# Kernel tuning notes

Hardware: AMD Instinct MI355X
Metric: run time of the kernel (lower is better)

Reference implementation:

```python
import jax, jax.numpy as jnp
import numpy as np

B, NL, C, H, W = 4, 2048, 128, 128, 128
N_PTS0, N_PTS1 = 32, 8
SCALE = N_PTS0 // N_PTS1  # MaxPool1d kernel/stride
FEATURE_DIM = 5
BN_EPS = 1e-5


def setup_inputs() -> dict:
    key = jax.random.key(0)
    ks = jax.random.split(key, 12)
    fm = jax.random.normal(ks[0], (B, C, H, W), dtype=jnp.float32)
    lines = jax.random.uniform(ks[1], (B, NL, 2, 2), dtype=jnp.float32) * 128.0
    P = C // 2
    s = 0.05
    return {
        "feature_map": fm,
        "lines": lines,
        # Bottleneck1D params (BatchNorm in eval mode: running_mean=0, running_var=1)
        "bn1_g": jnp.ones((C,), jnp.float32), "bn1_b": jnp.zeros((C,), jnp.float32),
        "conv1_w": jax.random.normal(ks[2], (P, C, 1), jnp.float32) * s,
        "conv1_b": jnp.zeros((P,), jnp.float32),
        "bn2_g": jnp.ones((P,), jnp.float32), "bn2_b": jnp.zeros((P,), jnp.float32),
        "conv2_w": jax.random.normal(ks[3], (P, P, 3), jnp.float32) * s,
        "conv2_b": jnp.zeros((P,), jnp.float32),
        "bn3_g": jnp.ones((P,), jnp.float32), "bn3_b": jnp.zeros((P,), jnp.float32),
        "conv3_w": jax.random.normal(ks[4], (C, P, 1), jnp.float32) * s,
        "conv3_b": jnp.zeros((C,), jnp.float32),
        # fc2: ReLU -> Linear(dim_loi*n_pts1 + 5, 4)
        "fc2_w": jax.random.normal(ks[5], (4, C * N_PTS1 + FEATURE_DIM), jnp.float32) * s,
        "fc2_b": jnp.zeros((4,), jnp.float32),
    }


def _bn(x, g, b):
    # eval-mode BatchNorm1d with running_mean=0, running_var=1
    return x * (g / jnp.sqrt(1.0 + BN_EPS))[None, :, None] + b[None, :, None]


def _conv1d(x, w, b, pad):
    y = jax.lax.conv_general_dilated(x, w, (1,), [(pad, pad)],
                                     dimension_numbers=("NCH", "OIH", "NCH"))
    return y + b[None, :, None]


def _loi_gather(fm, lines):
    # sample points along each line: [B, NL, N_PTS0, 2]
    lam = jnp.linspace(0.0, 1.0, N_PTS0, dtype=jnp.float32)[None, None, :, None]
    p = lines[:, :, 0:1, :] * lam + lines[:, :, 1:2, :] * (1.0 - lam) - 0.5
    p = p.reshape(B, -1, 2)                      # [B, NL*N_PTS0, 2]
    px, py = p[..., 0], p[..., 1]
    px0 = jnp.clip(jnp.floor(px), 0.0, 127.0)
    py0 = jnp.clip(jnp.floor(py), 0.0, 127.0)
    px1 = jnp.clip(px0 + 1.0, 0.0, 127.0)
    py1 = jnp.clip(py0 + 1.0, 0.0, 127.0)
    px0l, py0l = px0.astype(jnp.int32), py0.astype(jnp.int32)
    px1l, py1l = px1.astype(jnp.int32), py1.astype(jnp.int32)

    gather = jax.vmap(lambda f, yi, xi: f[:, yi, xi])  # [C, P] per image
    # weights exactly as in the torch source
    xp = (gather(fm, py0l, px0l) * ((px1 - px) * (py1 - py))[:, None, :]
          + gather(fm, py1l, px0l) * ((px - px0) * (py1 - py))[:, None, :]
          + gather(fm, py0l, px1l) * ((px1 - px) * (py - py0))[:, None, :]
          + gather(fm, py1l, px1l) * ((px - px0) * (py - py0))[:, None, :])
    # [B, C, NL*N_PTS0] -> [B*NL, C, N_PTS0]
    xp = xp.reshape(B, C, NL, N_PTS0).transpose(0, 2, 1, 3).reshape(B * NL, C, N_PTS0)
    return xp


def reference(feature_map, lines, bn1_g, bn1_b, conv1_w, conv1_b,
              bn2_g, bn2_b, conv2_w, conv2_b, bn3_g, bn3_b,
              conv3_w, conv3_b, fc2_w, fc2_b):
    xp = _loi_gather(feature_map, lines)               # [B*NL, C, N_PTS0]
    # MaxPool1d(SCALE, SCALE)
    x = xp.reshape(B * NL, C, N_PTS1, SCALE).max(axis=-1)
    # Bottleneck1D residual block
    y = jax.nn.relu(_bn(x, bn1_g, bn1_b))
    y = _conv1d(y, conv1_w, conv1_b, 0)
    y = jax.nn.relu(_bn(y, bn2_g, bn2_b))
    y = _conv1d(y, conv2_w, conv2_b, 1)
    y = jax.nn.relu(_bn(y, bn3_g, bn3_b))
    y = _conv1d(y, conv3_w, conv3_b, 0)
    x = x + y                                          # [B*NL, C, N_PTS1]
    # line geometry feature (use_cood=1, use_slop=1)
    xyu, xyv = lines[:, :, 0, :], lines[:, :, 1, :]
    u2v = jnp.sqrt(((xyu - xyv) ** 2).sum(-1, keepdims=True)).clip(min=1e-6)
    f = jnp.concatenate([xyu / 128.0, xyv / 128.0, u2v], axis=-1)
    f = f.reshape(B * NL, FEATURE_DIM)
    # concat + fc2 (ReLU -> Linear)
    x = jnp.concatenate([x.reshape(B * NL, C * N_PTS1), f], axis=1)
    logits = jax.nn.relu(x) @ fc2_w.T + fc2_b
    prob = jax.nn.softmax(logits, axis=1)
    return logits, prob
```

## Files before the change

### kernel.cpp

```cpp
#include <hip/hip_runtime.h>
#include <math.h>

#define BB 4
#define NLL 2048
#define CC 128
#define HH 128
#define WW 128
#define NPTS0 32
#define NPTS1 8
#define PP 64
#define FDIM 5
#define FCK (CC*NPTS1 + FDIM)

typedef __attribute__((ext_vector_type(8))) short bf16x8;
typedef __attribute__((ext_vector_type(4))) float f32x4;

__device__ __forceinline__ unsigned short f2bf(float f) {
    union { float f; unsigned u; } v; v.f = f;
    unsigned u = v.u;
    return (unsigned short)((u + 0x7fffu + ((u >> 16) & 1u)) >> 16);
}

__global__ __launch_bounds__(256)
void transpose_fm2(const float* __restrict__ fm, float* __restrict__ fmT) {
    __shared__ float tile[32 * 132];
    const int c0 = blockIdx.x * 32;
    const int by = blockIdx.y;
    const int b = by >> 7, y = by & 127;
    const int t = threadIdx.x;
    const float* src = fm + ((size_t)b * CC) * (HH * WW) + (size_t)y * WW;
    const int x4 = (t & 31) * 4;
    #pragma unroll
    for (int i = 0; i < 4; ++i) {
        int r = (t >> 5) + 8 * i;
        *(float4*)&tile[r * 132 + x4] =
            *(const float4*)&src[(size_t)(c0 + r) * (HH * WW) + x4];
    }
    __syncthreads();
    float* dst = fmT + (size_t)by * WW * CC + c0 + (t & 31);
    const int cr = (t & 31) * 132;
    #pragma unroll
    for (int i = 0; i < 16; ++i) {
        int x = (t >> 5) + 8 * i;
        dst[(size_t)x * CC] = tile[cr + x];
    }
}

__global__ __launch_bounds__(256)
void prep_weights(const float* __restrict__ w1, const float* __restrict__ w2,
                  const float* __restrict__ w3, unsigned short* __restrict__ W1b,
                  unsigned short* __restrict__ W2b, unsigned short* __restrict__ W3b) {
    int gid = blockIdx.x * 256 + threadIdx.x;
    if (gid < 8192) {
        W1b[gid] = f2bf(w1[gid]);
    } else if (gid < 20480) {
        int g = gid - 8192;
        int tt = g >> 12, r = g & 4095;
        int p = r >> 6, q = r & 63;
        W2b[tt * 4096 + p * 64 + q] = f2bf(w2[p * 192 + q * 3 + tt]);
    } else if (gid < 28672) {
        int g = gid - 20480;
        W3b[g] = f2bf(w3[g]);
    }
}

__global__ __launch_bounds__(256)
void line_mfma(const float* __restrict__ fmT,
               const float* __restrict__ lines,
               const float* __restrict__ bn1_g, const float* __restrict__ bn1_b,
               const unsigned short* __restrict__ W1b, const float* __restrict__ b1,
               const float* __restrict__ bn2_g, const float* __restrict__ bn2_b,
               const unsigned short* __restrict__ W2b, const float* __restrict__ b2,
               const float* __restrict__ bn3_g, const float* __restrict__ bn3_b,
               const unsigned short* __restrict__ W3b, const float* __restrict__ b3,
               const float* __restrict__ fcw,   const float* __restrict__ fcb,
               float* __restrict__ out) {
    __shared__ int   s_ix0[64], s_ix1[64], s_iy0[64], s_iy1[64];
    __shared__ float s_wA[64], s_wB[64], s_wC[64], s_wD[64];
    __shared__ float s_xs[16 * 128];
    __shared__ unsigned short s_ybn[16 * 136];
    __shared__ unsigned short s_z1[2 * 10 * 72];
    __shared__ unsigned short s_z2[16 * 72];
    __shared__ float s_feat[2][8];
    __shared__ float s_red[4 * 8];

    const int bx  = blockIdx.x;
    const int L0  = bx * 2;
    const int b   = bx >> 10;
    const int tid = threadIdx.x;
    const int lane = tid & 63;
    const int wv   = tid >> 6;
    const int quad = lane >> 4;
    const int l16  = lane & 15;
    const float inv_s = 1.0f / sqrtf(1.0f + 1e-5f);

    if (tid < 64) {
        int line = tid >> 5, pt = tid & 31;
        const float* ln = lines + (size_t)(L0 + line) * 4;
        float lam = (float)pt * (1.0f / 31.0f);
        float om  = 1.0f - lam;
        float px = ln[0] * lam + ln[2] * om - 0.5f;
        float py = ln[1] * lam + ln[3] * om - 0.5f;
        float px0 = fminf(fmaxf(floorf(px), 0.0f), 127.0f);
        float py0 = fminf(fmaxf(floorf(py), 0.0f), 127.0f);
        float px1 = fminf(px0 + 1.0f, 127.0f);
        float py1 = fminf(py0 + 1.0f, 127.0f);
        s_ix0[tid] = (int)px0; s_ix1[tid] = (int)px1;
        s_iy0[tid] = (int)py0; s_iy1[tid] = (int)py1;
        float ax = px1 - px, bxv = px - px0, ay = py1 - py, byv = py - py0;
        s_wA[tid] = ax  * ay;
        s_wB[tid] = bxv * ay;
        s_wC[tid] = ax  * byv;
        s_wD[tid] = bxv * byv;
    }
    if (tid >= 64 && tid < 66) {
        int line = tid - 64;
        const float* ln = lines + (size_t)(L0 + line) * 4;
        float ux = ln[0], uy = ln[1], vx = ln[2], vy = ln[3];
        float dx = ux - vx, dy = uy - vy;
        float d = fmaxf(sqrtf(dx * dx + dy * dy), 1e-6f);
        s_feat[line][0] = ux * (1.0f / 128.0f);
        s_feat[line][1] = uy * (1.0f / 128.0f);
        s_feat[line][2] = vx * (1.0f / 128.0f);
        s_feat[line][3] = vy * (1.0f / 128.0f);
        s_feat[line][4] = d;
    }
    if (tid < 128) {
        int line = tid >> 6, q = tid & 63;
        s_z1[line * 720 + 0 * 72 + q] = 0;
        s_z1[line * 720 + 9 * 72 + q] = 0;
    }
    __syncthreads();

    {
        int cq = tid & 31, k = tid >> 5;
        int c0 = cq * 4;
        const float* base = fmT + (size_t)b * (HH * WW * CC);
        #pragma unroll
        for (int line = 0; line < 2; ++line) {
            float4 acc;
            acc.x = -INFINITY; acc.y = -INFINITY; acc.z = -INFINITY; acc.w = -INFINITY;
            #pragma unroll
            for (int j = 0; j < 4; ++j) {
                int pt = line * 32 + k * 4 + j;
                int ix0 = s_ix0[pt], ix1 = s_ix1[pt];
                int iy0 = s_iy0[pt], iy1 = s_iy1[pt];
                float wA = s_wA[pt], wB = s_wB[pt], wC = s_wC[pt], wD = s_wD[pt];
                float4 vA = *(const float4*)(base + ((size_t)(iy0 * WW + ix0)) * CC + c0);
                float4 vB = *(const float4*)(base + ((size_t)(iy1 * WW + ix0)) * CC + c0);
                float4 vC = *(const float4*)(base + ((size_t)(iy0 * WW + ix1)) * CC + c0);
                float4 vD = *(const float4*)(base + ((size_t)(iy1 * WW + ix1)) * CC + c0);
                float4 v;
                v.x = wA * vA.x + wB * vB.x + wC * vC.x + wD * vD.x;
                v.y = wA * vA.y + wB * vB.y + wC * vC.y + wD * vD.y;
                v.z = wA * vA.z + wB * vB.z + wC * vC.z + wD * vD.z;
                v.w = wA * vA.w + wB * vB.w + wC * vC.w + wD * vD.w;
                acc.x = fmaxf(acc.x, v.x); acc.y = fmaxf(acc.y, v.y);
                acc.z = fmaxf(acc.z, v.z); acc.w = fmaxf(acc.w, v.w);
            }
            *(float4*)&s_xs[(line * 8 + k) * 128 + c0] = acc;
        }
    }
    __syncthreads();

    {
        int m = tid >> 4, c8 = (tid & 15) * 8;
        const float* xr = &s_xs[m * 128 + c8];
        float4 g0 = *(const float4*)(bn1_g + c8);
        float4 g1 = *(const float4*)(bn1_g + c8 + 4);
        float4 bb0 = *(const float4*)(bn1_b + c8);
        float4 bb1 = *(const float4*)(bn1_b + c8 + 4);
        const float* gg = (const float*)&g0;
        float gs[8] = {g0.x, g0.y, g0.z, g0.w, g1.x, g1.y, g1.z, g1.w};
        float bs[8] = {bb0.x, bb0.y, bb0.z, bb0.w, bb1.x, bb1.y, bb1.z, bb1.w};
        (void)gg;
        unsigned short* yr = &s_ybn[m * 136 + c8];
        #pragma unroll
        for (int i = 0; i < 8; ++i) {
            float v = fmaxf(xr[i] * (gs[i] * inv_s) + bs[i], 0.0f);
            yr[i] = f2bf(v);
        }
    }
    __syncthreads();

    {
        int n0 = wv * 16;
        f32x4 acc = {0.f, 0.f, 0.f, 0.f};
        #pragma unroll
        for (int kc = 0; kc < 4; ++kc) {
            bf16x8 a = *(const bf16x8*)&s_ybn[l16 * 136 + kc * 32 + quad * 8];
            bf16x8 bf = *(const bf16x8*)(W1b + (n0 + l16) * 128 + kc * 32 + quad * 8);
            acc = __builtin_amdgcn_mfma_f32_16x16x32_bf16(a, bf, acc, 0, 0, 0);
        }
        int p = n0 + l16;
        float s2 = bn2_g[p] * inv_s, bb2 = bn2_b[p], cb = b1[p];
        int line = quad >> 1;
        int kbase = (quad & 1) * 4;
        #pragma unroll
        for (int r = 0; r < 4; ++r) {
            float v = fmaxf((acc[r] + cb) * s2 + bb2, 0.0f);
            s_z1[line * 720 + (kbase + r + 1) * 72 + p] = f2bf(v);
        }
    }
    __syncthreads();

    {
        int n0 = wv * 16;
        f32x4 acc = {0.f, 0.f, 0.f, 0.f};
        int line = l16 >> 3, k = l16 & 7;
        #pragma unroll
        for (int t = 0; t < 3; ++t) {
            const unsigned short* arow = &s_z1[line * 720 + (k + t) * 72];
            #pragma unroll
            for (int kc = 0; kc < 2; ++kc) {
                bf16x8 a = *(const bf16x8*)&arow[kc * 32 + quad * 8];
                bf16x8 bf = *(const bf16x8*)(W2b + t * 4096 + (n0 + l16) * 64 + kc * 32 + quad * 8);
                acc = __builtin_amdgcn_mfma_f32_16x16x32_bf16(a, bf, acc, 0, 0, 0);
            }
        }
        int p = n0 + l16;
        float s3 = bn3_g[p] * inv_s, bb3 = bn3_b[p], cb = b2[p];
        #pragma unroll
        for (int r = 0; r < 4; ++r) {
            float v = fmaxf((acc[r] + cb) * s3 + bb3, 0.0f);
            s_z2[(quad * 4 + r) * 72 + p] = f2bf(v);
        }
    }
    __syncthreads();

    float p0 = 0.f, p1 = 0.f, p2 = 0.f, p3 = 0.f;
    {
        int kbase = (quad & 1) * 4;
        bf16x8 a0 = *(const bf16x8*)&s_z2[l16 * 72 + 0 * 32 + quad * 8];
        bf16x8 a1 = *(const bf16x8*)&s_z2[l16 * 72 + 1 * 32 + quad * 8];
        #pragma unroll
        for (int sub = 0; sub < 2; ++sub) {
            int n0 = wv * 32 + sub * 16;
            f32x4 acc = {0.f, 0.f, 0.f, 0.f};
            bf16x8 bf0 = *(const bf16x8*)(W3b + (n0 + l16) * 64 + 0 * 32 + quad * 8);
            bf16x8 bf1 = *(const bf16x8*)(W3b + (n0 + l16) * 64 + 1 * 32 + quad * 8);
            acc = __builtin_amdgcn_mfma_f32_16x16x32_bf16(a0, bf0, acc, 0, 0, 0);
            acc = __builtin_amdgcn_mfma_f32_16x16x32_bf16(a1, bf1, acc, 0, 0, 0);
            int c = n0 + l16;
            float cb = b3[c];
            #pragma unroll
            for (int r = 0; r < 4; ++r) {
                int m = quad * 4 + r;
                float v = fmaxf(s_xs[m * 128 + c] + acc[r] + cb, 0.0f);
                int idx = c * 8 + kbase + r;
                p0 = fmaf(v, fcw[0 * FCK + idx], p0);
                p1 = fmaf(v, fcw[1 * FCK + idx], p1);
                p2 = fmaf(v, fcw[2 * FCK + idx], p2);
                p3 = fmaf(v, fcw[3 * FCK + idx], p3);
            }
        }
    }
    #pragma unroll
    for (int off = 16; off >= 1; off >>= 1) {
        p0 += __shfl_down(p0, off);
        p1 += __shfl_down(p1, off);
        p2 += __shfl_down(p2, off);
        p3 += __shfl_down(p3, off);
    }
    if ((lane & 31) == 0) {
        int line = lane >> 5;
        s_red[wv * 8 + line * 4 + 0] = p0;
        s_red[wv * 8 + line * 4 + 1] = p1;
        s_red[wv * 8 + line * 4 + 2] = p2;
        s_red[wv * 8 + line * 4 + 3] = p3;
    }
    __syncthreads();

    if (tid < 2) {
        int line = tid;
        float lg[4];
        #pragma unroll
        for (int o = 0; o < 4; ++o) {
            lg[o] = fcb[o] + s_red[0 + line * 4 + o] + s_red[8 + line * 4 + o]
                  + s_red[16 + line * 4 + o] + s_red[24 + line * 4 + o];
        }
        #pragma unroll
        for (int j = 0; j < FDIM; ++j) {
            float fv = fmaxf(s_feat[line][j], 0.0f);
            #pragma unroll
            for (int o = 0; o < 4; ++o)
                lg[o] = fmaf(fv, fcw[o * FCK + 1024 + j], lg[o]);
        }
        float m = fmaxf(fmaxf(lg[0], lg[1]), fmaxf(lg[2], lg[3]));
        float e0 = expf(lg[0] - m), e1 = expf(lg[1] - m);
        float e2 = expf(lg[2] - m), e3 = expf(lg[3] - m);
        float inv = 1.0f / (e0 + e1 + e2 + e3);
        float* lo = out + (size_t)(L0 + line) * 4;
        lo[0] = lg[0]; lo[1] = lg[1]; lo[2] = lg[2]; lo[3] = lg[3];
        float* pr = out + (size_t)BB * NLL * 4 + (size_t)(L0 + line) * 4;
        pr[0] = e0 * inv; pr[1] = e1 * inv; pr[2] = e2 * inv; pr[3] = e3 * inv;
    }
}

template<bool TRANS>
__global__ __launch_bounds__(256)
void line_kernel_v1(const float* __restrict__ fm,
                    const float* __restrict__ lines,
                    const float* __restrict__ bn1_g, const float* __restrict__ bn1_b,
                    const float* __restrict__ w1,    const float* __restrict__ b1,
                    const float* __restrict__ bn2_g, const float* __restrict__ bn2_b,
                    const float* __restrict__ w2,    const float* __restrict__ b2,
                    const float* __restrict__ bn3_g, const float* __restrict__ bn3_b,
                    const float* __restrict__ w3,    const float* __restrict__ b3,
                    const float* __restrict__ fcw,   const float* __restrict__ fcb,
                    float* __restrict__ out) {
    __shared__ int   s_ix0[32], s_ix1[32], s_iy0[32], s_iy1[32];
    __shared__ float s_wA[32], s_wB[32], s_wC[32], s_wD[32];
    __shared__ float xs [8][132];
    __shared__ float ybn[8][132];
    __shared__ float z1 [64][12];
    __shared__ float z2 [64][8];
    __shared__ float s_feat[8];
    __shared__ float s_red[16];

    const int L   = blockIdx.x;
    const int b   = L / NLL;
    const int tid = threadIdx.x;
    const float inv_s = 1.0f / sqrtf(1.0f + 1e-5f);
    const float* ln = lines + (size_t)L * 4;

    if (tid < 32) {
        float lam = (float)tid * (1.0f / 31.0f);
        float om  = 1.0f - lam;
        float px = ln[0] * lam + ln[2] * om - 0.5f;
        float py = ln[1] * lam + ln[3] * om - 0.5f;
        float px0 = fminf(fmaxf(floorf(px), 0.0f), 127.0f);
        float py0 = fminf(fmaxf(floorf(py), 0.0f), 127.0f);
        float px1 = fminf(px0 + 1.0f, 127.0f);
        float py1 = fminf(py0 + 1.0f, 127.0f);
        s_ix0[tid] = (int)px0; s_ix1[tid] = (int)px1;
        s_iy0[tid] = (int)py0; s_iy1[tid] = (int)py1;
        float ax = px1 - px, bxv = px - px0, ay = py1 - py, byv = py - py0;
        s_wA[tid] = ax  * ay;  s_wB[tid] = bxv * ay;
        s_wC[tid] = ax  * byv; s_wD[tid] = bxv * byv;
    }
    if (tid == 0) {
        float ux = ln[0], uy = ln[1], vx = ln[2], vy = ln[3];
        float dx = ux - vx, dy = uy - vy;
        float d = fmaxf(sqrtf(dx * dx + dy * dy), 1e-6f);
        s_feat[0] = ux / 128.0f; s_feat[1] = uy / 128.0f;
        s_feat[2] = vx / 128.0f; s_feat[3] = vy / 128.0f;
        s_feat[4] = d;
    }
    __syncthreads();
    {
        int cq = tid & 31, k = tid >> 5, c0 = cq * 4;
        float4 acc;
        acc.x = -INFINITY; acc.y = -INFINITY; acc.z = -INFINITY; acc.w = -INFINITY;
        #pragma unroll
        for (int j = 0; j < 4; ++j) {
            int pt = k * 4 + j;
            int ix0 = s_ix0[pt], ix1 = s_ix1[pt];
            int iy0 = s_iy0[pt], iy1 = s_iy1[pt];
            float wA = s_wA[pt], wB = s_wB[pt], wC = s_wC[pt], wD = s_wD[pt];
            float4 vA, vB, vC, vD;
            if (TRANS) {
                const float* base = fm + (size_t)b * HH * WW * CC;
                vA = *(const float4*)(base + ((size_t)(iy0 * WW + ix0)) * CC + c0);
                vB = *(const float4*)(base + ((size_t)(iy1 * WW + ix0)) * CC + c0);
                vC = *(const float4*)(base + ((size_t)(iy0 * WW + ix1)) * CC + c0);
                vD = *(const float4*)(base + ((size_t)(iy1 * WW + ix1)) * CC + c0);
            } else {
                const float* base = fm + ((size_t)b * CC + c0) * HH * WW;
                int oA = iy0 * WW + ix0, oB = iy1 * WW + ix0;
                int oC = iy0 * WW + ix1, oD = iy1 * WW + ix1;
                vA.x = base[oA];           vB.x = base[oB];
                vC.x = base[oC];           vD.x = base[oD];
                vA.y = base[HH*WW + oA];   vB.y = base[HH*WW + oB];
                vC.y = base[HH*WW + oC];   vD.y = base[HH*WW + oD];
                vA.z = base[2*HH*WW + oA]; vB.z = base[2*HH*WW + oB];
                vC.z = base[2*HH*WW + oC]; vD.z = base[2*HH*WW + oD];
                vA.w = base[3*HH*WW + oA]; vB.w = base[3*HH*WW + oB];
                vC.w = base[3*HH*WW + oC]; vD.w = base[3*HH*WW + oD];
            }
            float4 v;
            v.x = wA * vA.x + wB * vB.x + wC * vC.x + wD * vD.x;
            v.y = wA * vA.y + wB * vB.y + wC * vC.y + wD * vD.y;
            v.z = wA * vA.z + wB * vB.z + wC * vC.z + wD * vD.z;
            v.w = wA * vA.w + wB * vB.w + wC * vC.w + wD * vD.w;
            acc.x = fmaxf(acc.x, v.x); acc.y = fmaxf(acc.y, v.y);
            acc.z = fmaxf(acc.z, v.z); acc.w = fmaxf(acc.w, v.w);
        }
        *(float4*)(&xs[k][c0]) = acc;
    }
    __syncthreads();
    for (int e = tid; e < 1024; e += 256) {
        int k = e >> 7, c = e & 127;
        ybn[k][c] = fmaxf(xs[k][c] * (bn1_g[c] * inv_s) + bn1_b[c], 0.0f);
    }
    __syncthreads();
    if (tid < 64) { z1[tid][0] = 0.0f; z1[tid][9] = 0.0f; }
    {
        int p = tid >> 2, kq = tid & 3;
        const float* wrow = w1 + p * 128;
        float a0a = 0.f, a0b = 0.f, a1a = 0.f, a1b = 0.f;
        #pragma unroll 8
        for (int c = 0; c < 128; c += 4) {
            float4 w  = *(const float4*)(wrow + c);
            float4 ya = *(const float4*)(&ybn[kq][c]);
            float4 yb = *(const float4*)(&ybn[kq + 4][c]);
            a0a = fmaf(w.x, ya.x, a0a); a0b = fmaf(w.y, ya.y, a0b);
            a0a = fmaf(w.z, ya.z, a0a); a0b = fmaf(w.w, ya.w, a0b);
            a1a = fmaf(w.x, yb.x, a1a); a1b = fmaf(w.y, yb.y, a1b);
            a1a = fmaf(w.z, yb.z, a1a); a1b = fmaf(w.w, yb.w, a1b);
        }
        float s2 = bn2_g[p] * inv_s, bb = bn2_b[p], cb = b1[p];
        z1[p][1 + kq]     = fmaxf((a0a + a0b + cb) * s2 + bb, 0.0f);
        z1[p][1 + kq + 4] = fmaxf((a1a + a1b + cb) * s2 + bb, 0.0f);
    }
    __syncthreads();
    {
        int p = tid >> 2, kq = tid & 3;
        const float* wrow = w2 + p * 192;
        float acc0 = 0.f, acc1 = 0.f;
        #pragma unroll 4
        for (int q = 0; q < 64; ++q) {
            float w0 = wrow[q * 3 + 0], w1v = wrow[q * 3 + 1], w2v = wrow[q * 3 + 2];
            const float* zr = &z1[q][0];
            acc0 = fmaf(w0, zr[kq], acc0);
            acc0 = fmaf(w1v, zr[kq + 1], acc0);
            acc0 = fmaf(w2v, zr[kq + 2], acc0);
            acc1 = fmaf(w0, zr[kq + 4], acc1);
            acc1 = fmaf(w1v, zr[kq + 5], acc1);
            acc1 = fmaf(w2v, zr[kq + 6], acc1);
        }
        float s3 = bn3_g[p] * inv_s, bb = bn3_b[p], cb = b2[p];
        z2[p][kq]     = fmaxf((acc0 + cb) * s3 + bb, 0.0f);
        z2[p][kq + 4] = fmaxf((acc1 + cb) * s3 + bb, 0.0f);
    }
    __syncthreads();
    float part0 = 0.f, part1 = 0.f, part2 = 0.f, part3 = 0.f;
    {
        int c = tid >> 1, kq = tid & 1;
        const float* wrow = w3 + c * 64;
        float acc[4] = {0.f, 0.f, 0.f, 0.f};
        #pragma unroll 8
        for (int q = 0; q < 64; ++q) {
            float w = wrow[q];
            acc[0] = fmaf(w, z2[q][kq], acc[0]);
            acc[1] = fmaf(w, z2[q][kq + 2], acc[1]);
            acc[2] = fmaf(w, z2[q][kq + 4], acc[2]);
            acc[3] = fmaf(w, z2[q][kq + 6], acc[3]);
        }
        float cb = b3[c];
        #pragma unroll
        for (int i = 0; i < 4; ++i) {
            int k = kq + 2 * i;
            float v = fmaxf(xs[k][c] + acc[i] + cb, 0.0f);
            int idx = c * 8 + k;
            part0 = fmaf(v, fcw[0 * FCK + idx], part0);
            part1 = fmaf(v, fcw[1 * FCK + idx], part1);
            part2 = fmaf(v, fcw[2 * FCK + idx], part2);
            part3 = fmaf(v, fcw[3 * FCK + idx], part3);
        }
    }
    #pragma unroll
    for (int off = 32; off > 0; off >>= 1) {
        part0 += __shfl_down(part0, off);
        part1 += __shfl_down(part1, off);
        part2 += __shfl_down(part2, off);
        part3 += __shfl_down(part3, off);
    }
    if ((tid & 63) == 0) {
        int w = tid >> 6;
        s_red[w * 4 + 0] = part0; s_red[w * 4 + 1] = part1;
        s_red[w * 4 + 2] = part2; s_red[w * 4 + 3] = part3;
    }
    __syncthreads();
    if (tid == 0) {
        float lg[4];
        #pragma unroll
        for (int o = 0; o < 4; ++o)
            lg[o] = fcb[o] + s_red[o] + s_red[4 + o] + s_red[8 + o] + s_red[12 + o];
        #pragma unroll
        for (int j = 0; j < FDIM; ++j) {
            float fv = fmaxf(s_feat[j], 0.0f);
            #pragma unroll
            for (int o = 0; o < 4; ++o)
                lg[o] = fmaf(fv, fcw[o * FCK + 1024 + j], lg[o]);
        }
        float m = fmaxf(fmaxf(lg[0], lg[1]), fmaxf(lg[2], lg[3]));
        float e0 = expf(lg[0] - m), e1 = expf(lg[1] - m);
        float e2 = expf(lg[2] - m), e3 = expf(lg[3] - m);
        float inv = 1.0f / (e0 + e1 + e2 + e3);
        float* lo = out + (size_t)L * 4;
        lo[0] = lg[0]; lo[1] = lg[1]; lo[2] = lg[2]; lo[3] = lg[3];
        float* pr = out + (size_t)BB * NLL * 4 + (size_t)L * 4;
        pr[0] = e0 * inv; pr[1] = e1 * inv; pr[2] = e2 * inv; pr[3] = e3 * inv;
    }
}

extern "C" void kernel_launch(void* const* d_in, const int* in_sizes, int n_in,
                              void* d_out, int out_size, void* d_ws, size_t ws_size,
                              hipStream_t stream) {
    const float* fm     = (const float*)d_in[0];
    const float* lines  = (const float*)d_in[1];
    const float* bn1_g  = (const float*)d_in[2];
    const float* bn1_b  = (const float*)d_in[3];
    const float* w1     = (const float*)d_in[4];
    const float* b1     = (const float*)d_in[5];
    const float* bn2_g  = (const float*)d_in[6];
    const float* bn2_b  = (const float*)d_in[7];
    const float* w2     = (const float*)d_in[8];
    const float* b2     = (const float*)d_in[9];
    const float* bn3_g  = (const float*)d_in[10];
    const float* bn3_b  = (const float*)d_in[11];
    const float* w3     = (const float*)d_in[12];
    const float* b3     = (const float*)d_in[13];
    const float* fcw    = (const float*)d_in[14];
    const float* fcb    = (const float*)d_in[15];
    float* out = (float*)d_out;

    const size_t fmT_bytes = (size_t)BB * HH * WW * CC * sizeof(float);
    const size_t wb_bytes  = 57344;

    if (ws_size >= fmT_bytes + wb_bytes) {
        float* fmT = (float*)d_ws;
        unsigned short* W1b = (unsigned short*)((char*)d_ws + fmT_bytes);
        unsigned short* W2b = W1b + 8192;
        unsigned short* W3b = W2b + 12288;
        dim3 tg(CC / 32, BB * HH);
        transpose_fm2<<<tg, 256, 0, stream>>>(fm, fmT);
        prep_weights<<<112, 256, 0, stream>>>(w1, w2, w3, W1b, W2b, W3b);
        line_mfma<<<BB * NLL / 2, 256, 0, stream>>>(
            fmT, lines, bn1_g, bn1_b, W1b, b1, bn2_g, bn2_b, W2b, b2,
            bn3_g, bn3_b, W3b, b3, fcw, fcb, out);
    } else if (ws_size >= fmT_bytes) {
        float* fmT = (float*)d_ws;
        dim3 tg(CC / 32, BB * HH);
        transpose_fm2<<<tg, 256, 0, stream>>>(fm, fmT);
        line_kernel_v1<true><<<BB * NLL, 256, 0, stream>>>(
            fmT, lines, bn1_g, bn1_b, w1, b1, bn2_g, bn2_b, w2, b2,
            bn3_g, bn3_b, w3, b3, fcw, fcb, out);
    } else {
        line_kernel_v1<false><<<BB * NLL, 256, 0, stream>>>(
            fm, lines, bn1_g, bn1_b, w1, b1, bn2_g, bn2_b, w2, b2,
            bn3_g, bn3_b, w3, b3, fcw, fcb, out);
    }
}
```

Measured before the change: 167.4 us.

## Store transposed feature map in bf16 and gather 8-channel bf16 vectors

The transpose kernel now converts the feature map to bf16 while transposing to channel-last, using a swizzled shared tile and 64-column halves. The line kernel gathers bilinear corners as 8-wide bf16 vectors using precomputed flat offsets, then converts back to float for interpolation and max-pooling. This halves the bytes written by the transpose and read by the gather. The cost is reduced precision of the sampled features before pooling.

```diff
diff --git a/kernel.cpp b/kernel.cpp
--- a/kernel.cpp
+++ b/kernel.cpp
@@ -20,29 +20,41 @@
     unsigned u = v.u;
     return (unsigned short)((u + 0x7fffu + ((u >> 16) & 1u)) >> 16);
 }
+__device__ __forceinline__ float bf2f(unsigned short s) {
+    union { unsigned u; float f; } v; v.u = ((unsigned)s) << 16;
+    return v.f;
+}
 
 __global__ __launch_bounds__(256)
-void transpose_fm2(const float* __restrict__ fm, float* __restrict__ fmT) {
-    __shared__ float tile[32 * 132];
-    const int c0 = blockIdx.x * 32;
-    const int by = blockIdx.y;
+void transpose_fm3(const float* __restrict__ fm, unsigned short* __restrict__ fmT) {
+    __shared__ unsigned short tile[128 * 72];
+    const int by = blockIdx.x >> 1;
+    const int xh = blockIdx.x & 1;
     const int b = by >> 7, y = by & 127;
     const int t = threadIdx.x;
-    const float* src = fm + ((size_t)b * CC) * (HH * WW) + (size_t)y * WW;
-    const int x4 = (t & 31) * 4;
+    const float* src = fm + ((size_t)b * CC) * (HH * WW) + (size_t)y * WW + xh * 64;
+    const int x4 = (t & 15) * 4;
+    const int r0 = t >> 4;
     #pragma unroll
-    for (int i = 0; i < 4; ++i) {
-        int r = (t >> 5) + 8 * i;
-        *(float4*)&tile[r * 132 + x4] =
-            *(const float4*)&src[(size_t)(c0 + r) * (HH * WW) + x4];
-    }
-    __syncthreads();
-    float* dst = fmT + (size_t)by * WW * CC + c0 + (t & 31);
-    const int cr = (t & 31) * 132;
+    for (int i = 0; i < 8; ++i) {
+        int r = r0 + 16 * i;
+        float4 v = *(const float4*)&src[(size_t)r * (HH * WW) + x4];
+        ushort4 u;
+        u.x = f2bf(v.x); u.y = f2bf(v.y); u.z = f2bf(v.z); u.w = f2bf(v.w);
+        *(ushort4*)&tile[r * 72 + (x4 ^ (r & 28))] = u;
+    }
+    __syncthreads();
+    unsigned short* dst = fmT + ((size_t)by * WW + xh * 64) * CC;
+    const int c4 = (t & 31) * 4;
     #pragma unroll
-    for (int i = 0; i < 16; ++i) {
+    for (int i = 0; i < 8; ++i) {
         int x = (t >> 5) + 8 * i;
-        dst[(size_t)x * CC] = tile[cr + x];
+        ushort4 u;
+        u.x = tile[(c4 + 0) * 72 + (x ^ ((c4 + 0) & 28))];
+        u.y = tile[(c4 + 1) * 72 + (x ^ ((c4 + 1) & 28))];
+        u.z = tile[(c4 + 2) * 72 + (x ^ ((c4 + 2) & 28))];
+        u.w = tile[(c4 + 3) * 72 + (x ^ ((c4 + 3) & 28))];
+        *(ushort4*)&dst[(size_t)x * CC + c4] = u;
     }
 }
 
@@ -65,7 +77,7 @@
 }
 
 __global__ __launch_bounds__(256)
-void line_mfma(const float* __restrict__ fmT,
+void line_mfma(const unsigned short* __restrict__ fmT,
                const float* __restrict__ lines,
                const float* __restrict__ bn1_g, const float* __restrict__ bn1_b,
                const unsigned short* __restrict__ W1b, const float* __restrict__ b1,
@@ -75,7 +87,7 @@
                const unsigned short* __restrict__ W3b, const float* __restrict__ b3,
                const float* __restrict__ fcw,   const float* __restrict__ fcb,
                float* __restrict__ out) {
-    __shared__ int   s_ix0[64], s_ix1[64], s_iy0[64], s_iy1[64];
+    __shared__ int   s_oA[64], s_oB[64], s_oC[64], s_oD[64];
     __shared__ float s_wA[64], s_wB[64], s_wC[64], s_wD[64];
     __shared__ float s_xs[16 * 128];
     __shared__ unsigned short s_ybn[16 * 136];
@@ -105,8 +117,11 @@
         float py0 = fminf(fmaxf(floorf(py), 0.0f), 127.0f);
         float px1 = fminf(px0 + 1.0f, 127.0f);
         float py1 = fminf(py0 + 1.0f, 127.0f);
-        s_ix0[tid] = (int)px0; s_ix1[tid] = (int)px1;
-        s_iy0[tid] = (int)py0; s_iy1[tid] = (int)py1;
+        int ix0 = (int)px0, ix1 = (int)px1, iy0 = (int)py0, iy1 = (int)py1;
+        s_oA[tid] = (iy0 * WW + ix0) * CC;
+        s_oB[tid] = (iy1 * WW + ix0) * CC;
+        s_oC[tid] = (iy0 * WW + ix1) * CC;
+        s_oD[tid] = (iy1 * WW + ix1) * CC;
         float ax = px1 - px, bxv = px - px0, ay = py1 - py, byv = py - py0;
         s_wA[tid] = ax  * ay;
         s_wB[tid] = bxv * ay;
@@ -133,53 +148,46 @@
     __syncthreads();
 
     {
-        int cq = tid & 31, k = tid >> 5;
-        int c0 = cq * 4;
-        const float* base = fmT + (size_t)b * (HH * WW * CC);
-        #pragma unroll
-        for (int line = 0; line < 2; ++line) {
-            float4 acc;
-            acc.x = -INFINITY; acc.y = -INFINITY; acc.z = -INFINITY; acc.w = -INFINITY;
+        int tl = tid >> 4;
+        int line = tl >> 3, k = tl & 7;
+        int c8 = (tid & 15) * 8;
+        const unsigned short* base = fmT + (size_t)b * (HH * WW * CC) + c8;
+        float acc[8];
+        #pragma unroll
+        for (int i = 0; i < 8; ++i) acc[i] = -INFINITY;
+        #pragma unroll
+        for (int j = 0; j < 4; ++j) {
+            int pt = line * 32 + k * 4 + j;
+            bf16x8 rA = *(const bf16x8*)(base + s_oA[pt]);
+            bf16x8 rB = *(const bf16x8*)(base + s_oB[pt]);
+            bf16x8 rC = *(const bf16x8*)(base + s_oC[pt]);
+            bf16x8 rD = *(const bf16x8*)(base + s_oD[pt]);
+            float wA = s_wA[pt], wB = s_wB[pt], wC = s_wC[pt], wD = s_wD[pt];
             #pragma unroll
-            for (int j = 0; j < 4; ++j) {
-                int pt = line * 32 + k * 4 + j;
-                int ix0 = s_ix0[pt], ix1 = s_ix1[pt];
-                int iy0 = s_iy0[pt], iy1 = s_iy1[pt];
-                float wA = s_wA[pt], wB = s_wB[pt], wC = s_wC[pt], wD = s_wD[pt];
-                float4 vA = *(const float4*)(base + ((size_t)(iy0 * WW + ix0)) * CC + c0);
-                float4 vB = *(const float4*)(base + ((size_t)(iy1 * WW + ix0)) * CC + c0);
-                float4 vC = *(const float4*)(base + ((size_t)(iy0 * WW + ix1)) * CC + c0);
-                float4 vD = *(const float4*)(base + ((size_t)(iy1 * WW + ix1)) * CC + c0);
-                float4 v;
-                v.x = wA * vA.x + wB * vB.x + wC * vC.x + wD * vD.x;
-                v.y = wA * vA.y + wB * vB.y + wC * vC.y + wD * vD.y;
-                v.z = wA * vA.z + wB * vB.z + wC * vC.z + wD * vD.z;
-                v.w = wA * vA.w + wB * vB.w + wC * vC.w + wD * vD.w;
-                acc.x = fmaxf(acc.x, v.x); acc.y = fmaxf(acc.y, v.y);
-                acc.z = fmaxf(acc.z, v.z); acc.w = fmaxf(acc.w, v.w);
+            for (int i = 0; i < 8; ++i) {
+                float v = wA * bf2f((unsigned short)rA[i])
+                        + wB * bf2f((unsigned short)rB[i])
+                        + wC * bf2f((unsigned short)rC[i])
+                        + wD * bf2f((unsigned short)rD[i]);
+                acc[i] = fmaxf(acc[i], v);
             }
-            *(float4*)&s_xs[(line * 8 + k) * 128 + c0] = acc;
-        }
+        }
+        float* xr = &s_xs[tl * 128 + c8];
+        #pragma unroll
+        for (int i = 0; i < 8; ++i) xr[i] = acc[i];
     }
     __syncthreads();
 
     {
         int m = tid >> 4, c8 = (tid & 15) * 8;
         const float* xr = &s_xs[m * 128 + c8];
-        float4 g0 = *(const float4*)(bn1_g + c8);
-        float4 g1 = *(const float4*)(bn1_g + c8 + 4);
-        float4 bb0 = *(const float4*)(bn1_b + c8);
-        float4 bb1 = *(const float4*)(bn1_b + c8 + 4);
-        const float* gg = (const float*)&g0;
-        float gs[8] = {g0.x, g0.y, g0.z, g0.w, g1.x, g1.y, g1.z, g1.w};
-        float bs[8] = {bb0.x, bb0.y, bb0.z, bb0.w, bb1.x, bb1.y, bb1.z, bb1.w};
-        (void)gg;
-        unsigned short* yr = &s_ybn[m * 136 + c8];
+        bf16x8 pack;
         #pragma unroll
         for (int i = 0; i < 8; ++i) {
-            float v = fmaxf(xr[i] * (gs[i] * inv_s) + bs[i], 0.0f);
-            yr[i] = f2bf(v);
-        }
+            float v = fmaxf(xr[i] * (bn1_g[c8 + i] * inv_s) + bn1_b[c8 + i], 0.0f);
+            pack[i] = (short)f2bf(v);
+        }
+        *(bf16x8*)&s_ybn[m * 136 + c8] = pack;
     }
     __syncthreads();
 
@@ -294,6 +302,31 @@
         lo[0] = lg[0]; lo[1] = lg[1]; lo[2] = lg[2]; lo[3] = lg[3];
         float* pr = out + (size_t)BB * NLL * 4 + (size_t)(L0 + line) * 4;
         pr[0] = e0 * inv; pr[1] = e1 * inv; pr[2] = e2 * inv; pr[3] = e3 * inv;
+    }
+}
+
+__global__ __launch_bounds__(256)
+void transpose_fm2(const float* __restrict__ fm, float* __restrict__ fmT) {
+    __shared__ float tile[32 * 132];
+    const int c0 = blockIdx.x * 32;
+    const int by = blockIdx.y;
+    const int b = by >> 7, y = by & 127;
+    const int t = threadIdx.x;
+    const float* src = fm + ((size_t)b * CC) * (HH * WW) + (size_t)y * WW;
+    const int x4 = (t & 31) * 4;
+    #pragma unroll
+    for (int i = 0; i < 4; ++i) {
+        int r = (t >> 5) + 8 * i;
+        *(float4*)&tile[r * 132 + x4] =
+            *(const float4*)&src[(size_t)(c0 + r) * (HH * WW) + x4];
+    }
+    __syncthreads();
+    float* dst = fmT + (size_t)by * WW * CC + c0 + (t & 31);
+    const int cr = (t & 31) * 132;
+    #pragma unroll
+    for (int i = 0; i < 16; ++i) {
+        int x = (t >> 5) + 8 * i;
+        dst[(size_t)x * CC] = tile[cr + x];
     }
 }
 
@@ -516,21 +549,21 @@
     const float* fcb    = (const float*)d_in[15];
     float* out = (float*)d_out;
 
-    const size_t fmT_bytes = (size_t)BB * HH * WW * CC * sizeof(float);
-    const size_t wb_bytes  = 57344;
-
-    if (ws_size >= fmT_bytes + wb_bytes) {
-        float* fmT = (float*)d_ws;
-        unsigned short* W1b = (unsigned short*)((char*)d_ws + fmT_bytes);
+    const size_t fmTb_bytes = (size_t)BB * HH * WW * CC * sizeof(unsigned short);
+    const size_t fmTf_bytes = (size_t)BB * HH * WW * CC * sizeof(float);
+    const size_t wb_bytes   = 57344;
+
+    if (ws_size >= fmTb_bytes + wb_bytes) {
+        unsigned short* fmT = (unsigned short*)d_ws;
+        unsigned short* W1b = (unsigned short*)((char*)d_ws + fmTb_bytes);
         unsigned short* W2b = W1b + 8192;
         unsigned short* W3b = W2b + 12288;
-        dim3 tg(CC / 32, BB * HH);
-        transpose_fm2<<<tg, 256, 0, stream>>>(fm, fmT);
         prep_weights<<<112, 256, 0, stream>>>(w1, w2, w3, W1b, W2b, W3b);
+        transpose_fm3<<<BB * HH * 2, 256, 0, stream>>>(fm, fmT);
         line_mfma<<<BB * NLL / 2, 256, 0, stream>>>(
             fmT, lines, bn1_g, bn1_b, W1b, b1, bn2_g, bn2_b, W2b, b2,
             bn3_g, bn3_b, W3b, b3, fcw, fcb, out);
-    } else if (ws_size >= fmT_bytes) {
+    } else if (ws_size >= fmTf_bytes) {
         float* fmT = (float*)d_ws;
         dim3 tg(CC / 32, BB * HH);
         transpose_fm2<<<tg, 256, 0, stream>>>(fm, fmT);
```

Result: faster. 154.3 us (-7.8%).
